# Optimization experiments

Hardware: AMD Instinct MI355X
Metric: run time of the kernel (lower is better)

Reference implementation:

```python
import jax, jax.numpy as jnp
import numpy as np

B, V, C, M, CM, D, OUT = 16, 16, 64, 32, 16, 128, 600
VOCAB = {"cond": 4000, "proc": 2000, "drug": 600, "lab_item": 700, "lab_value": 2000, "inj_item": 400, "inj_value": 2000}


def _gru(x, Wih, Whh, bih, bhh):
    """Batch-first torch-style GRU. x: [N,T,D] -> (outputs [N,T,D], h_T [N,D])."""
    Dh = Whh.shape[1]

    def step(h, xt):
        gi = xt @ Wih.T + bih
        gh = h @ Whh.T + bhh
        ir, iz, ig = jnp.split(gi, 3, axis=-1)
        hr, hz, hg = jnp.split(gh, 3, axis=-1)
        r = jax.nn.sigmoid(ir + hr)
        z = jax.nn.sigmoid(iz + hz)
        n = jnp.tanh(ig + r * hg)
        h = (1.0 - z) * n + z * h
        return h, h

    h0 = jnp.zeros((x.shape[0], Dh), x.dtype)
    hT, ys = jax.lax.scan(step, h0, jnp.swapaxes(x, 0, 1))
    return jnp.swapaxes(ys, 0, 1), hT


def _hetero_mp(feats, Wself, Wmsg):
    """Heterogeneous message passing over node types on the fully-connected
    monitor<->visit-feature bipartite pattern: each node type combines a self
    transform with a transformed mean of the other node types, then ReLU.
    feats: list of [N,D]; Wself/Wmsg: [T,D,D]."""
    stacked = jnp.stack(feats)  # [T,N,D]
    total = jnp.sum(stacked, axis=0)
    T = stacked.shape[0]
    outs = []
    for t in range(T):
        others = (total - stacked[t]) / (T - 1)
        outs.append(jax.nn.relu(stacked[t] @ Wself[t] + others @ Wmsg[t]))
    return outs


def _forward(codes_cond, codes_proc, codes_drug, codes_lab_item, codes_lab_value,
             codes_inj_item, codes_inj_value, weight, age,
             emb_cond, emb_proc, emb_drug, emb_lab_item, emb_lab_value,
             emb_inj_item, emb_inj_value,
             mgru_Wih, mgru_Whh, mgru_bih, mgru_bhh,
             vgru_Wih, vgru_Whh, vgru_bih, vgru_bhh,
             gnn_Wself, gnn_Wmsg,
             fc_weight_W, fc_weight_b, fc_age_W, fc_age_b,
             fc_patient_W, fc_patient_b):
    # ---- visit-event features: embedding lookup + sum-pool over codes ----
    vis = {}
    for k, codes, emb in (("cond", codes_cond, emb_cond),
                          ("proc", codes_proc, emb_proc),
                          ("drug", codes_drug, emb_drug)):
        vis[k] = jnp.sum(emb[codes], axis=2)  # [B,V,D]
    visit_keys = ("cond", "proc", "drug")

    # ---- monitor-event pairs: (item * value) embeddings, GNN, two-level GRU ----
    pairs = (
        (codes_lab_item, codes_lab_value, emb_lab_item, emb_lab_value, "lab_item", (0, 2, 3, 4)),
        (codes_inj_item, codes_inj_value, emb_inj_item, emb_inj_value, "inj_item", (1, 2, 3, 4)),
    )
    hid = {}
    for p, (ci, cv, ei, ev, ikey, gidx) in enumerate(pairs):
        mon = jnp.sum(ei[ci] * ev[cv], axis=3)  # [B,V,M,D]
        feats = [mon.reshape(-1, D)]  # monitor node type, [B*V*M, D]
        for k in visit_keys:  # visit features repeated across monitors
            feats.append(jnp.broadcast_to(vis[k][:, :, None, :], (B, V, M, D)).reshape(-1, D))
        outs = _hetero_mp(feats, gnn_Wself[p], gnn_Wmsg[p])
        for t, k in enumerate((ikey,) + visit_keys):
            g = gidx[t]
            # monitor-level GRU over the M monitors of each visit
            o, _ = _gru(outs[t].reshape(B * V, M, D), mgru_Wih[g], mgru_Whh[g], mgru_bih[g], mgru_bhh[g])
            last = o[:, -1, :].reshape(B, V, D)  # last monitor state per visit
            # visit-level GRU (source uses visit_gru[feature_key1] for all keys)
            _, h = _gru(last, vgru_Wih[p], vgru_Whh[p], vgru_bih[p], vgru_bhh[p])
            hid[k] = h if k not in hid else hid[k] + h

    # ---- weight / age scalar features ----
    for k, x, W, b, vi in (("weight", weight, fc_weight_W, fc_weight_b, 2),
                           ("age", age, fc_age_W, fc_age_b, 3)):
        mask = (x != 0.0)[..., None]  # [B,V,1]
        xe = (x[..., None] * W[:, 0] + b) * mask  # Linear(1->D) then zero-mask
        _, h = _gru(xe, vgru_Wih[vi], vgru_Whh[vi], vgru_bih[vi], vgru_bhh[vi])
        hid[k] = h

    # ---- concat in dict-insertion order, then ReLU + Linear head ----
    pe = jnp.concatenate([hid["lab_item"], hid["cond"], hid["proc"], hid["drug"],
                          hid["inj_item"], hid["weight"], hid["age"]], axis=-1)  # [B, 7D]
    return jax.nn.relu(pe) @ fc_patient_W.T + fc_patient_b  # [B, OUT]


def setup_inputs() -> dict:
    key = jax.random.key(0)
    ks = iter(jax.random.split(key, 64))

    def nrm(shape, s=0.1):
        return (jax.random.normal(next(ks), shape) * s).astype(jnp.float32)

    def emb_table(vsz):
        t = nrm((vsz, D), 1.0)
        return t.at[0].set(0.0)  # padding_idx=0 row is zero

    inp = {}
    inp["codes_cond"] = jax.random.randint(next(ks), (B, V, C), 0, VOCAB["cond"], dtype=jnp.int32)
    inp["codes_proc"] = jax.random.randint(next(ks), (B, V, C), 0, VOCAB["proc"], dtype=jnp.int32)
    inp["codes_drug"] = jax.random.randint(next(ks), (B, V, C), 0, VOCAB["drug"], dtype=jnp.int32)
    inp["codes_lab_item"] = jax.random.randint(next(ks), (B, V, M, CM), 0, VOCAB["lab_item"], dtype=jnp.int32)
    inp["codes_lab_value"] = jax.random.randint(next(ks), (B, V, M, CM), 0, VOCAB["lab_value"], dtype=jnp.int32)
    inp["codes_inj_item"] = jax.random.randint(next(ks), (B, V, M, CM), 0, VOCAB["inj_item"], dtype=jnp.int32)
    inp["codes_inj_value"] = jax.random.randint(next(ks), (B, V, M, CM), 0, VOCAB["inj_value"], dtype=jnp.int32)
    inp["weight"] = jax.random.uniform(next(ks), (B, V), minval=0.1, maxval=1.0, dtype=jnp.float32)
    inp["age"] = jax.random.uniform(next(ks), (B, V), minval=0.1, maxval=1.0, dtype=jnp.float32)
    inp["emb_cond"] = emb_table(VOCAB["cond"])
    inp["emb_proc"] = emb_table(VOCAB["proc"])
    inp["emb_drug"] = emb_table(VOCAB["drug"])
    inp["emb_lab_item"] = emb_table(VOCAB["lab_item"])
    inp["emb_lab_value"] = emb_table(VOCAB["lab_value"])
    inp["emb_inj_item"] = emb_table(VOCAB["inj_item"])
    inp["emb_inj_value"] = emb_table(VOCAB["inj_value"])
    inp["mgru_Wih"] = nrm((5, 3 * D, D))
    inp["mgru_Whh"] = nrm((5, 3 * D, D))
    inp["mgru_bih"] = nrm((5, 3 * D))
    inp["mgru_bhh"] = nrm((5, 3 * D))
    inp["vgru_Wih"] = nrm((4, 3 * D, D))
    inp["vgru_Whh"] = nrm((4, 3 * D, D))
    inp["vgru_bih"] = nrm((4, 3 * D))
    inp["vgru_bhh"] = nrm((4, 3 * D))
    inp["gnn_Wself"] = nrm((2, 4, D, D))
    inp["gnn_Wmsg"] = nrm((2, 4, D, D))
    inp["fc_weight_W"] = nrm((D, 1))
    inp["fc_weight_b"] = nrm((D,))
    inp["fc_age_W"] = nrm((D, 1))
    inp["fc_age_b"] = nrm((D,))
    inp["fc_patient_W"] = nrm((OUT, 7 * D))
    inp["fc_patient_b"] = nrm((OUT,))
    return inp


def reference(codes_cond, codes_proc, codes_drug, codes_lab_item, codes_lab_value,
              codes_inj_item, codes_inj_value, weight, age,
              emb_cond, emb_proc, emb_drug, emb_lab_item, emb_lab_value,
              emb_inj_item, emb_inj_value,
              mgru_Wih, mgru_Whh, mgru_bih, mgru_bhh,
              vgru_Wih, vgru_Whh, vgru_bih, vgru_bhh,
              gnn_Wself, gnn_Wmsg,
              fc_weight_W, fc_weight_b, fc_age_W, fc_age_b,
              fc_patient_W, fc_patient_b):
    return _forward(codes_cond, codes_proc, codes_drug, codes_lab_item, codes_lab_value,
                    codes_inj_item, codes_inj_value, weight, age,
                    emb_cond, emb_proc, emb_drug, emb_lab_item, emb_lab_value,
                    emb_inj_item, emb_inj_value,
                    mgru_Wih, mgru_Whh, mgru_bih, mgru_bhh,
                    vgru_Wih, vgru_Whh, vgru_bih, vgru_bhh,
                    gnn_Wself, gnn_Wmsg,
                    fc_weight_W, fc_weight_b, fc_age_W, fc_age_b,
                    fc_patient_W, fc_patient_b)
```

## Files before the change

### kernel.cpp

```cpp
#include <hip/hip_runtime.h>
#include <math.h>

#define B_   16
#define V_   16
#define C_   64
#define M_   32
#define CM_  16
#define D_   128
#define OUT_ 600
#define NSEQ 256
#define NROW 8192

typedef __attribute__((ext_vector_type(8))) short bf16x8;
typedef __attribute__((ext_vector_type(4))) short bf16x4;
typedef __attribute__((ext_vector_type(4))) float f32x4;

__device__ __forceinline__ unsigned short f2bf(float x) {
  union { float f; unsigned u; } v; v.f = x;
  unsigned r = v.u + 0x7fff + ((v.u >> 16) & 1);
  return (unsigned short)(r >> 16);
}
__device__ __forceinline__ float bf2f(short s) {
  union { unsigned u; float f; } v;
  v.u = ((unsigned)(unsigned short)s) << 16;
  return v.f;
}
__device__ __forceinline__ float fsig(float x)  { return __fdividef(1.f, 1.f + __expf(-x)); }
__device__ __forceinline__ float ftanh(float x) { return 1.f - 2.f*__fdividef(1.f, __expf(2.f*x) + 1.f); }

__device__ __forceinline__ void ldsbar() {
  asm volatile("s_waitcnt lgkmcnt(0)" ::: "memory");
  __builtin_amdgcn_s_barrier();
  asm volatile("" ::: "memory");
}

constexpr int OFF_VISB  = 98304;
constexpr int OFF_MONB  = 147456;
constexpr int OFF_W12T  = 2244608;
constexpr int OFF_WIHB  = 2375680;
constexpr int OFF_WIHTV = 2498560;
constexpr int OFF_XE    = 2695168;
constexpr int OFF_LAST  = 27926528;
constexpr int OFF_VH    = 29171712;

__global__ __launch_bounds__(256) void k_prepvis(
    const float* __restrict__ Wself, const float* __restrict__ Wmsg,
    const float* __restrict__ mWih,  const float* __restrict__ vWih,
    const float* __restrict__ wgt,   const float* __restrict__ age,
    const float* __restrict__ fwW,   const float* __restrict__ fwB,
    const float* __restrict__ faW,   const float* __restrict__ faB,
    const int* __restrict__ cc, const int* __restrict__ cp, const int* __restrict__ cd,
    const float* __restrict__ ec, const float* __restrict__ ep, const float* __restrict__ ed,
    const int* __restrict__ cli, const int* __restrict__ clv,
    const int* __restrict__ cii, const int* __restrict__ civ,
    const float* __restrict__ eli, const float* __restrict__ elv,
    const float* __restrict__ eii, const float* __restrict__ eiv,
    short* __restrict__ w12t, short* __restrict__ wihb,
    float* __restrict__ wihTv, float* __restrict__ xe,
    short* __restrict__ visb, short* __restrict__ monb)
{
  int bx = blockIdx.x, tid = threadIdx.x;
  if (bx < 1024) {
    int lin = bx*256 + tid;
    int pt = lin >> 15, rem = lin & 32767;
    int n = rem >> 8, k = rem & 255;
    float v;
    if (k < 128) v = Wself[pt*16384 + k*128 + n] - Wmsg[pt*16384 + k*128 + n]*(1.f/3.f);
    else         v = Wmsg[pt*16384 + (k-128)*128 + n]*(1.f/3.f);
    w12t[lin] = (short)f2bf(v);
  } else if (bx < 1984) {
    int lin = (bx-1024)*256 + tid;
    wihb[lin] = (short)f2bf(mWih[lin]);
  } else if (bx < 2752) {
    int lin = (bx-1984)*256 + tid;
    int g = lin / 49152, rem2 = lin % 49152;
    int k = rem2 / 384, j = rem2 % 384;
    wihTv[lin] = vWih[g*49152 + j*128 + k];
  } else if (bx < 3008) {
    int lin = (bx-2752)*256 + tid;
    int which = lin >> 15, rem2 = lin & 32767;
    int n = rem2 >> 7, d = rem2 & 127;
    float x  = which ? age[n] : wgt[n];
    float Wv = which ? faW[d] : fwW[d];
    float bb = which ? faB[d] : fwB[d];
    xe[lin] = (x != 0.0f) ? (x*Wv + bb) : 0.0f;
  } else if (bx < 3392) {
    int idx = (bx-3008)*256 + tid;
    int type = idx >> 15;
    int r = idx & 32767;
    int bv = r >> 7, d = r & 127;
    const int*   codes = (type==0) ? cc : (type==1) ? cp : cd;
    const float* emb   = (type==0) ? ec : (type==1) ? ep : ed;
    float acc = 0.f;
    for (int c = 0; c < C_; ++c) {
      int code = codes[bv*C_ + c];
      acc += emb[code*D_ + d];
    }
    visb[(type*NSEQ + bv)*D_ + d] = (short)f2bf(acc);
  } else {
    int rowid = (bx-3392)*2 + (tid >> 7);
    int p = rowid >> 13, bvm = rowid & 8191;
    int d = tid & 127;
    const int* ci = p ? cii : cli;  const int* cv = p ? civ : clv;
    const float* ei = p ? eii : eli; const float* ev = p ? eiv : elv;
    float acc = 0.f;
    #pragma unroll
    for (int c2 = 0; c2 < CM_; ++c2) {
      int iv = ci[bvm*CM_ + c2];
      int vv = cv[bvm*CM_ + c2];
      acc += ei[iv*D_ + d] * ev[vv*D_ + d];
    }
    monb[((size_t)p*NROW + bvm)*D_ + d] = (short)f2bf(acc);
  }
}

__global__ __launch_bounds__(512, 1) void k_ggru(
    const short* __restrict__ monb, const short* __restrict__ visb,
    const short* __restrict__ w12t, const short* __restrict__ wihb,
    const float* __restrict__ mWhh, const float* __restrict__ mbih,
    const float* __restrict__ mbhh, float* __restrict__ last)
{
  const int run  = blockIdx.x >> 4;
  const int pair = blockIdx.x & 15;
  const int p = run >> 2, t = run & 3;
  const int g = (run % 4 == 0) ? (run / 4) : (run % 4 + 1);
  const int tid = threadIdx.x;
  const int w = tid >> 6;
  const int lane = tid & 63;
  const int c = lane & 15, q = lane >> 4;
  const int j = w*16 + c;

  __shared__ short hb[2][4][16][40];
  __shared__ __align__(16) short Ys[2][16][136];
  __shared__ __align__(16) short Xl[2][4096];

  for (int idx = tid; idx < 2*4*16*40; idx += 512)
    ((short*)hb)[idx] = 0;

  bf16x8 bW12[8];
  #pragma unroll
  for (int kt = 0; kt < 8; ++kt)
    bW12[kt] = *(const bf16x8*)(w12t + (size_t)run*32768 + (size_t)(w*16+c)*256 + kt*32 + q*8);

  bf16x8 bWih[3][4];
  #pragma unroll
  for (int gate = 0; gate < 3; ++gate)
    #pragma unroll
    for (int kt = 0; kt < 4; ++kt)
      bWih[gate][kt] = *(const bf16x8*)(wihb + ((size_t)g*384 + gate*128 + j)*128 + kt*32 + q*8);

  bf16x8 bWhh[3][4];
  #pragma unroll
  for (int gate = 0; gate < 3; ++gate) {
    const float* wp = mWhh + ((size_t)g*384 + gate*128 + j)*128 + q*8;
    #pragma unroll
    for (int kt = 0; kt < 4; ++kt) {
      float4 lo = *(const float4*)(wp + kt*32);
      float4 hi = *(const float4*)(wp + kt*32 + 4);
      bf16x8 tt;
      tt[0]=(short)f2bf(lo.x); tt[1]=(short)f2bf(lo.y); tt[2]=(short)f2bf(lo.z); tt[3]=(short)f2bf(lo.w);
      tt[4]=(short)f2bf(hi.x); tt[5]=(short)f2bf(hi.y); tt[6]=(short)f2bf(hi.z); tt[7]=(short)f2bf(hi.w);
      bWhh[gate][kt] = tt;
    }
  }
  const float bs0 = mbih[g*384 +       j] + mbhh[g*384 +       j];
  const float bs1 = mbih[g*384 + 128 + j] + mbhh[g*384 + 128 + j];
  const float bi2 = mbih[g*384 + 256 + j];
  const float bh2 = mbhh[g*384 + 256 + j];

  const int xr_ = tid >> 5, xu = tid & 31;
  const int bv = pair*16 + xr_;
  const bool istot = (xu >= 16);
  const short* fsrc;
  int fstride;
  float vsf[8] = {0.f,0.f,0.f,0.f,0.f,0.f,0.f,0.f};
  if (!istot) {
    if (t == 0) { fsrc = monb + ((size_t)p*NROW + (size_t)bv*32)*128 + xu*8; fstride = 128; }
    else        { fsrc = visb + ((size_t)(t-1)*NSEQ + bv)*128 + xu*8;        fstride = 0;   }
  } else {
    fsrc = monb + ((size_t)p*NROW + (size_t)bv*32)*128 + (xu-16)*8;          fstride = 128;
    #pragma unroll
    for (int i = 0; i < 8; ++i)
      vsf[i] = bf2f(visb[(0*NSEQ + bv)*128 + (xu-16)*8 + i])
             + bf2f(visb[(1*NSEQ + bv)*128 + (xu-16)*8 + i])
             + bf2f(visb[(2*NSEQ + bv)*128 + (xu-16)*8 + i]);
  }
  auto fixtot = [&](bf16x8 x) -> bf16x8 {
    if (istot) {
      #pragma unroll
      for (int i = 0; i < 8; ++i) x[i] = (short)f2bf(bf2f(x[i]) + vsf[i]);
    }
    return x;
  };
  const int xdofs = xr_*256 + (((xu*16) ^ ((xr_&7)<<4)) >> 1);
  short* xdst0 = &Xl[0][xdofs];
  short* xdst1 = &Xl[1][xdofs];

  {
    bf16x8 x0 = fixtot(*(const bf16x8*)fsrc);
    bf16x8 x1 = fixtot(*(const bf16x8*)(fsrc + fstride));
    *(bf16x8*)xdst0 = x0;
    *(bf16x8*)xdst1 = x1;
  }
  float hf[4] = {0.f,0.f,0.f,0.f};
  const int ktw = w >> 1;
  const int kkw = (w & 1)*16 + c;
  ldsbar();

  {
    const char* xbase = (const char*)&Xl[0][0];
    f32x4 accY = (f32x4){0.f,0.f,0.f,0.f};
    #pragma unroll
    for (int kt = 0; kt < 8; ++kt) {
      bf16x8 aX = *(const bf16x8*)(xbase + c*512 + ((kt*64 + q*16) ^ ((c&7)<<4)));
      accY = __builtin_amdgcn_mfma_f32_16x16x32_bf16(aX, bW12[kt], accY, 0, 0, 0);
    }
    #pragma unroll
    for (int reg = 0; reg < 4; ++reg)
      Ys[0][q*4 + reg][w*16 + c] = (short)f2bf(fmaxf(accY[reg], 0.f));
  }
  ldsbar();

  #pragma unroll 1
  for (int m = 0; m < 32; ++m) {
    const int cur = m & 1, nxt = cur ^ 1;

    bf16x8 xnext;
    if (m < 30) xnext = *(const bf16x8*)(fsrc + (size_t)(m+2)*fstride);

    f32x4 accY = (f32x4){0.f,0.f,0.f,0.f};
    if (m < 31) {
      const char* xbase = (const char*)&Xl[nxt][0];
      #pragma unroll
      for (int kt = 0; kt < 8; ++kt) {
        bf16x8 aX = *(const bf16x8*)(xbase + c*512 + ((kt*64 + q*16) ^ ((c&7)<<4)));
        accY = __builtin_amdgcn_mfma_f32_16x16x32_bf16(aX, bW12[kt], accY, 0, 0, 0);
      }
    }

    bf16x8 ah[4], a2[4];
    #pragma unroll
    for (int kt = 0; kt < 4; ++kt) {
      ah[kt] = *(const bf16x8*)&hb[cur][kt][c][q*8];
      a2[kt] = *(const bf16x8*)&Ys[cur][c][kt*32 + q*8];
    }
    f32x4 acc0 = (f32x4){0.f,0.f,0.f,0.f};
    f32x4 acc1 = (f32x4){0.f,0.f,0.f,0.f};
    f32x4 aG2  = (f32x4){0.f,0.f,0.f,0.f};
    f32x4 aH2  = (f32x4){0.f,0.f,0.f,0.f};
    #pragma unroll
    for (int kt = 0; kt < 4; ++kt) {
      acc0 = __builtin_amdgcn_mfma_f32_16x16x32_bf16(ah[kt], bWhh[0][kt], acc0, 0, 0, 0);
      acc1 = __builtin_amdgcn_mfma_f32_16x16x32_bf16(ah[kt], bWhh[1][kt], acc1, 0, 0, 0);
      aH2  = __builtin_amdgcn_mfma_f32_16x16x32_bf16(ah[kt], bWhh[2][kt], aH2,  0, 0, 0);
    }
    #pragma unroll
    for (int kt = 0; kt < 4; ++kt) {
      acc0 = __builtin_amdgcn_mfma_f32_16x16x32_bf16(a2[kt], bWih[0][kt], acc0, 0, 0, 0);
      acc1 = __builtin_amdgcn_mfma_f32_16x16x32_bf16(a2[kt], bWih[1][kt], acc1, 0, 0, 0);
      aG2  = __builtin_amdgcn_mfma_f32_16x16x32_bf16(a2[kt], bWih[2][kt], aG2,  0, 0, 0);
    }

    if (m < 31) {
      #pragma unroll
      for (int reg = 0; reg < 4; ++reg)
        Ys[nxt][q*4 + reg][w*16 + c] = (short)f2bf(fmaxf(accY[reg], 0.f));
    }
    if (m < 30) *(bf16x8*)(cur ? xdst1 : xdst0) = fixtot(xnext);

    #pragma unroll
    for (int reg = 0; reg < 4; ++reg) {
      float rr = fsig(acc0[reg] + bs0);
      float zz = fsig(acc1[reg] + bs1);
      float nn = ftanh(aG2[reg] + bi2 + rr*(aH2[reg] + bh2));
      float hnew = (1.f - zz)*nn + zz*hf[reg];
      hf[reg] = hnew;
      hb[nxt][ktw][q*4 + reg][kkw] = (short)f2bf(hnew);
    }
    ldsbar();
  }

  #pragma unroll
  for (int reg = 0; reg < 4; ++reg)
    last[((size_t)run*NSEQ + pair*16 + q*4 + reg)*D_ + j] = hf[reg];
}

__global__ __launch_bounds__(768) void k_vgru(
    const float* __restrict__ last, const float* __restrict__ xe,
    const float* __restrict__ wihTv, const float* __restrict__ vbih,
    const float* __restrict__ vWhh, const float* __restrict__ vbhh,
    float* __restrict__ vh)
{
  int run = blockIdx.x >> 4, b = blockIdx.x & 15;
  int tid = threadIdx.x;
  int vidx = (run < 4) ? 0 : (run < 8) ? 1 : (run - 6);

  __shared__ float Xs[16][128];
  __shared__ float giL[16*384];
  __shared__ __align__(16) float hsv[128];
  __shared__ float gh[384];

  const float* X = (run < 8) ? (last + ((size_t)run*NSEQ + b*16)*D_)
                             : (xe + ((size_t)(run-8)*NSEQ + b*16)*D_);
  for (int idx = tid; idx < 2048; idx += 768)
    ((float*)Xs)[idx] = X[idx];
  if (tid < 128) hsv[tid] = 0.f;
  __syncthreads();

  {
    int half = (tid >= 384) ? 1 : 0;
    int j = tid - half*384;
    float accv[8];
    float bias = vbih[vidx*384 + j];
    #pragma unroll
    for (int s = 0; s < 8; ++s) accv[s] = bias;
    const float* W = wihTv + vidx*49152 + j;
    #pragma unroll 4
    for (int k = 0; k < 128; ++k) {
      float wv = W[k*384];
      #pragma unroll
      for (int s = 0; s < 8; ++s) accv[s] += Xs[half*8 + s][k] * wv;
    }
    #pragma unroll
    for (int s = 0; s < 8; ++s)
      giL[(half*8 + s)*384 + j] = accv[s];
  }

  int j = tid >> 1, kh = tid & 1;
  float w[64];
  const float4* wrow = (const float4*)(vWhh + (vidx*384 + j)*128 + kh*64);
  #pragma unroll
  for (int k4 = 0; k4 < 16; ++k4) {
    float4 t4 = wrow[k4];
    w[4*k4] = t4.x; w[4*k4+1] = t4.y; w[4*k4+2] = t4.z; w[4*k4+3] = t4.w;
  }
  float bj = vbhh[vidx*384 + j];
  __syncthreads();

  #pragma unroll 1
  for (int v = 0; v < 16; ++v) {
    const float4* h4 = (const float4*)(hsv + kh*64);
    float p0 = 0.f, p1 = 0.f;
    #pragma unroll
    for (int k4 = 0; k4 < 8; ++k4) {
      float4 u0 = h4[k4], u1 = h4[k4+8];
      p0 += w[4*k4   ]*u0.x + w[4*k4+1 ]*u0.y + w[4*k4+2 ]*u0.z + w[4*k4+3 ]*u0.w;
      p1 += w[4*k4+32]*u1.x + w[4*k4+33]*u1.y + w[4*k4+34]*u1.z + w[4*k4+35]*u1.w;
    }
    float part = p0 + p1;
    part += __shfl_xor(part, 1);
    if (kh == 0) gh[j] = bj + ((j < 256) ? giL[v*384 + j] : 0.f) + part;
    __syncthreads();
    if (tid < 128) {
      float r = fsig(gh[tid]);
      float z = fsig(gh[tid+128]);
      float gin = giL[v*384 + 256 + tid];
      float n = ftanh(gin + r*gh[tid+256]);
      hsv[tid] = (1.f - z)*n + z*hsv[tid];
    }
    __syncthreads();
  }
  if (tid < 128) vh[(run*16 + b)*D_ + tid] = hsv[tid];
}

__global__ __launch_bounds__(256) void k_head(
    const float* __restrict__ vh, const float* __restrict__ Wp,
    const float* __restrict__ bp, float* __restrict__ out)
{
  const int o = blockIdx.x;
  const int tid = threadIdx.x;
  const int b = tid & 15, kc = tid >> 4;
  const int a1[7] = {0,1,2,3,4,8,9};
  const int a2[7] = {-1,5,6,7,-1,-1,-1};
  const float4* wb = (const float4*)(Wp + (size_t)o*896 + kc*56);
  float acc = 0.f;
  #pragma unroll
  for (int i = 0; i < 14; ++i) {
    int cc2 = kc*56 + i*4;
    int s = cc2 >> 7, d0 = cc2 & 127;
    float4 a = *(const float4*)(vh + (a1[s]*16 + b)*D_ + d0);
    int s2 = a2[s];
    if (s2 >= 0) {
      float4 a2v = *(const float4*)(vh + (s2*16 + b)*D_ + d0);
      a.x += a2v.x; a.y += a2v.y; a.z += a2v.z; a.w += a2v.w;
    }
    a.x = fmaxf(a.x, 0.f); a.y = fmaxf(a.y, 0.f);
    a.z = fmaxf(a.z, 0.f); a.w = fmaxf(a.w, 0.f);
    float4 ww = wb[i];
    acc += a.x*ww.x + a.y*ww.y + a.z*ww.z + a.w*ww.w;
  }
  __shared__ float red[16][17];
  red[kc][b] = acc;
  __syncthreads();
  if (tid < 16) {
    float s = 0.f;
    #pragma unroll
    for (int k = 0; k < 16; ++k) s += red[k][tid];
    out[tid*OUT_ + o] = s + bp[o];
  }
}

extern "C" void kernel_launch(void* const* d_in, const int* in_sizes, int n_in,
                              void* d_out, int out_size, void* d_ws, size_t ws_size,
                              hipStream_t stream)
{
  (void)in_sizes; (void)n_in; (void)out_size; (void)ws_size;
  const int*   cc   = (const int*)  d_in[0];
  const int*   cp   = (const int*)  d_in[1];
  const int*   cd   = (const int*)  d_in[2];
  const int*   cli  = (const int*)  d_in[3];
  const int*   clv  = (const int*)  d_in[4];
  const int*   cii  = (const int*)  d_in[5];
  const int*   civ  = (const int*)  d_in[6];
  const float* wgt  = (const float*)d_in[7];
  const float* age  = (const float*)d_in[8];
  const float* ec   = (const float*)d_in[9];
  const float* ep   = (const float*)d_in[10];
  const float* ed   = (const float*)d_in[11];
  const float* eli  = (const float*)d_in[12];
  const float* elv  = (const float*)d_in[13];
  const float* eii  = (const float*)d_in[14];
  const float* eiv  = (const float*)d_in[15];
  const float* mWih = (const float*)d_in[16];
  const float* mWhh = (const float*)d_in[17];
  const float* mbih = (const float*)d_in[18];
  const float* mbhh = (const float*)d_in[19];
  const float* vWih = (const float*)d_in[20];
  const float* vWhh = (const float*)d_in[21];
  const float* vbih = (const float*)d_in[22];
  const float* vbhh = (const float*)d_in[23];
  const float* Wself= (const float*)d_in[24];
  const float* Wmsg = (const float*)d_in[25];
  const float* fwW  = (const float*)d_in[26];
  const float* fwB  = (const float*)d_in[27];
  const float* faW  = (const float*)d_in[28];
  const float* faB  = (const float*)d_in[29];
  const float* Wp   = (const float*)d_in[30];
  const float* bp   = (const float*)d_in[31];
  float* out = (float*)d_out;
  float* ws  = (float*)d_ws;

  short* visb  = (short*)(ws + OFF_VISB);
  short* monb  = (short*)(ws + OFF_MONB);
  short* w12t  = (short*)(ws + OFF_W12T);
  short* wihb  = (short*)(ws + OFF_WIHB);
  float* wihTv = ws + OFF_WIHTV;
  float* xe    = ws + OFF_XE;
  float* last  = ws + OFF_LAST;
  float* vh    = ws + OFF_VH;

  k_prepvis<<<11584, 256, 0, stream>>>(Wself, Wmsg, mWih, vWih, wgt, age,
                                       fwW, fwB, faW, faB,
                                       cc, cp, cd, ec, ep, ed,
                                       cli, clv, cii, civ, eli, elv, eii, eiv,
                                       w12t, wihb, wihTv, xe, visb, monb);
  k_ggru<<<128, 512, 0, stream>>>(monb, visb, w12t, wihb,
                                  mWhh, mbih, mbhh, last);
  k_vgru<<<160, 768, 0, stream>>>(last, xe, wihTv, vbih, vWhh, vbhh, vh);
  k_head<<<600, 256, 0, stream>>>(vh, Wp, bp, out);
}
```

Baseline: 251.3 us.

## Hoist time-invariant visit-feature GEMM terms out of monitor GRU loop

The per-step input projection splits into a part that depends on the monitor row and a part from visit features that stays fixed over the 32 steps. The fixed part (visit sum times the message weights, plus the self term when the target is a visit type) is now computed once into a precomputed accumulator before the loop. Each step then runs a K=128 MFMA over only the monitor row instead of K=256, and only half the threads stage X into a half-sized LDS buffer. In exchange, the t==0 run loads its own Wself weights from global memory as strided fp32 reads at startup, and rounding changes slightly because bf16 sums are formed differently.

```diff
diff --git a/kernel.cpp b/kernel.cpp
--- a/kernel.cpp
+++ b/kernel.cpp
@@ -117,8 +117,9 @@
 __global__ __launch_bounds__(512, 1) void k_ggru(
     const short* __restrict__ monb, const short* __restrict__ visb,
     const short* __restrict__ w12t, const short* __restrict__ wihb,
-    const float* __restrict__ mWhh, const float* __restrict__ mbih,
-    const float* __restrict__ mbhh, float* __restrict__ last)
+    const float* __restrict__ Wself, const float* __restrict__ mWhh,
+    const float* __restrict__ mbih, const float* __restrict__ mbhh,
+    float* __restrict__ last)
 {
   const int run  = blockIdx.x >> 4;
   const int pair = blockIdx.x & 15;
@@ -132,7 +133,7 @@
 
   __shared__ short hb[2][4][16][40];
   __shared__ __align__(16) short Ys[2][16][136];
-  __shared__ __align__(16) short Xl[2][4096];
+  __shared__ __align__(16) short Xl[2][2048];
 
   for (int idx = tid; idx < 2*4*16*40; idx += 512)
     ((short*)hb)[idx] = 0;
@@ -140,7 +141,48 @@
   bf16x8 bW12[8];
   #pragma unroll
   for (int kt = 0; kt < 8; ++kt)
-    bW12[kt] = *(const bf16x8*)(w12t + (size_t)run*32768 + (size_t)(w*16+c)*256 + kt*32 + q*8);
+    bW12[kt] = *(const bf16x8*)(w12t + (size_t)run*32768 + (size_t)j*256 + kt*32 + q*8);
+
+  bf16x8 bWs[4];
+  if (t == 0) {
+    const float* wsp = Wself + (size_t)run*16384 + j;
+    #pragma unroll
+    for (int kt = 0; kt < 4; ++kt) {
+      bf16x8 tt;
+      #pragma unroll
+      for (int i = 0; i < 8; ++i)
+        tt[i] = (short)f2bf(wsp[(kt*32 + q*8 + i)*128]);
+      bWs[kt] = tt;
+    }
+  } else {
+    #pragma unroll
+    for (int kt = 0; kt < 4; ++kt) bWs[kt] = bW12[kt+4];
+  }
+
+  f32x4 Cpre = (f32x4){0.f,0.f,0.f,0.f};
+  {
+    const int bvc = pair*16 + c;
+    #pragma unroll
+    for (int kt = 0; kt < 4; ++kt) {
+      const int ko = kt*32 + q*8;
+      bf16x8 v0 = *(const bf16x8*)(visb + (size_t)(0*NSEQ + bvc)*128 + ko);
+      bf16x8 v1 = *(const bf16x8*)(visb + (size_t)(1*NSEQ + bvc)*128 + ko);
+      bf16x8 v2 = *(const bf16x8*)(visb + (size_t)(2*NSEQ + bvc)*128 + ko);
+      bf16x8 vs;
+      #pragma unroll
+      for (int i = 0; i < 8; ++i)
+        vs[i] = (short)f2bf(bf2f(v0[i]) + bf2f(v1[i]) + bf2f(v2[i]));
+      Cpre = __builtin_amdgcn_mfma_f32_16x16x32_bf16(vs, bW12[kt+4], Cpre, 0, 0, 0);
+    }
+    if (t > 0) {
+      #pragma unroll
+      for (int kt = 0; kt < 4; ++kt) {
+        const int ko = kt*32 + q*8;
+        bf16x8 fv = *(const bf16x8*)(visb + (size_t)((t-1)*NSEQ + bvc)*128 + ko);
+        Cpre = __builtin_amdgcn_mfma_f32_16x16x32_bf16(fv, bW12[kt], Cpre, 0, 0, 0);
+      }
+    }
+  }
 
   bf16x8 bWih[3][4];
   #pragma unroll
@@ -168,39 +210,17 @@
   const float bi2 = mbih[g*384 + 256 + j];
   const float bh2 = mbhh[g*384 + 256 + j];
 
-  const int xr_ = tid >> 5, xu = tid & 31;
+  const bool stg = (tid < 256);
+  const int xr_ = (tid >> 4) & 15, xu = tid & 15;
   const int bv = pair*16 + xr_;
-  const bool istot = (xu >= 16);
-  const short* fsrc;
-  int fstride;
-  float vsf[8] = {0.f,0.f,0.f,0.f,0.f,0.f,0.f,0.f};
-  if (!istot) {
-    if (t == 0) { fsrc = monb + ((size_t)p*NROW + (size_t)bv*32)*128 + xu*8; fstride = 128; }
-    else        { fsrc = visb + ((size_t)(t-1)*NSEQ + bv)*128 + xu*8;        fstride = 0;   }
-  } else {
-    fsrc = monb + ((size_t)p*NROW + (size_t)bv*32)*128 + (xu-16)*8;          fstride = 128;
-    #pragma unroll
-    for (int i = 0; i < 8; ++i)
-      vsf[i] = bf2f(visb[(0*NSEQ + bv)*128 + (xu-16)*8 + i])
-             + bf2f(visb[(1*NSEQ + bv)*128 + (xu-16)*8 + i])
-             + bf2f(visb[(2*NSEQ + bv)*128 + (xu-16)*8 + i]);
-  }
-  auto fixtot = [&](bf16x8 x) -> bf16x8 {
-    if (istot) {
-      #pragma unroll
-      for (int i = 0; i < 8; ++i) x[i] = (short)f2bf(bf2f(x[i]) + vsf[i]);
-    }
-    return x;
-  };
-  const int xdofs = xr_*256 + (((xu*16) ^ ((xr_&7)<<4)) >> 1);
+  const short* fsrc = monb + ((size_t)p*NROW + (size_t)bv*32)*128 + xu*8;
+  const int xdofs = xr_*128 + (((xu*16) ^ ((xr_&7)<<4)) >> 1);
   short* xdst0 = &Xl[0][xdofs];
   short* xdst1 = &Xl[1][xdofs];
 
-  {
-    bf16x8 x0 = fixtot(*(const bf16x8*)fsrc);
-    bf16x8 x1 = fixtot(*(const bf16x8*)(fsrc + fstride));
-    *(bf16x8*)xdst0 = x0;
-    *(bf16x8*)xdst1 = x1;
+  if (stg) {
+    *(bf16x8*)xdst0 = *(const bf16x8*)fsrc;
+    *(bf16x8*)xdst1 = *(const bf16x8*)(fsrc + 128);
   }
   float hf[4] = {0.f,0.f,0.f,0.f};
   const int ktw = w >> 1;
@@ -209,11 +229,11 @@
 
   {
     const char* xbase = (const char*)&Xl[0][0];
-    f32x4 accY = (f32x4){0.f,0.f,0.f,0.f};
-    #pragma unroll
-    for (int kt = 0; kt < 8; ++kt) {
-      bf16x8 aX = *(const bf16x8*)(xbase + c*512 + ((kt*64 + q*16) ^ ((c&7)<<4)));
-      accY = __builtin_amdgcn_mfma_f32_16x16x32_bf16(aX, bW12[kt], accY, 0, 0, 0);
+    f32x4 accY = Cpre;
+    #pragma unroll
+    for (int kt = 0; kt < 4; ++kt) {
+      bf16x8 aX = *(const bf16x8*)(xbase + c*256 + ((kt*64 + q*16) ^ ((c&7)<<4)));
+      accY = __builtin_amdgcn_mfma_f32_16x16x32_bf16(aX, bWs[kt], accY, 0, 0, 0);
     }
     #pragma unroll
     for (int reg = 0; reg < 4; ++reg)
@@ -226,15 +246,15 @@
     const int cur = m & 1, nxt = cur ^ 1;
 
     bf16x8 xnext;
-    if (m < 30) xnext = *(const bf16x8*)(fsrc + (size_t)(m+2)*fstride);
-
-    f32x4 accY = (f32x4){0.f,0.f,0.f,0.f};
+    if (stg && m < 30) xnext = *(const bf16x8*)(fsrc + (size_t)(m+2)*128);
+
+    f32x4 accY = Cpre;
     if (m < 31) {
       const char* xbase = (const char*)&Xl[nxt][0];
       #pragma unroll
-      for (int kt = 0; kt < 8; ++kt) {
-        bf16x8 aX = *(const bf16x8*)(xbase + c*512 + ((kt*64 + q*16) ^ ((c&7)<<4)));
-        accY = __builtin_amdgcn_mfma_f32_16x16x32_bf16(aX, bW12[kt], accY, 0, 0, 0);
+      for (int kt = 0; kt < 4; ++kt) {
+        bf16x8 aX = *(const bf16x8*)(xbase + c*256 + ((kt*64 + q*16) ^ ((c&7)<<4)));
+        accY = __builtin_amdgcn_mfma_f32_16x16x32_bf16(aX, bWs[kt], accY, 0, 0, 0);
       }
     }
 
@@ -266,7 +286,7 @@
       for (int reg = 0; reg < 4; ++reg)
         Ys[nxt][q*4 + reg][w*16 + c] = (short)f2bf(fmaxf(accY[reg], 0.f));
     }
-    if (m < 30) *(bf16x8*)(cur ? xdst1 : xdst0) = fixtot(xnext);
+    if (stg && m < 30) *(bf16x8*)(cur ? xdst1 : xdst0) = xnext;
 
     #pragma unroll
     for (int reg = 0; reg < 4; ++reg) {
@@ -454,7 +474,7 @@
                                        cc, cp, cd, ec, ep, ed,
                                        cli, clv, cii, civ, eli, elv, eii, eiv,
                                        w12t, wihb, wihTv, xe, visb, monb);
-  k_ggru<<<128, 512, 0, stream>>>(monb, visb, w12t, wihb,
+  k_ggru<<<128, 512, 0, stream>>>(monb, visb, w12t, wihb, Wself,
                                   mWhh, mbih, mbhh, last);
   k_vgru<<<160, 768, 0, stream>>>(last, xe, wihTv, vbih, vWhh, vbhh, vh);
   k_head<<<600, 256, 0, stream>>>(vh, Wp, bp, out);
```

Result: faster. 244.8 us (-2.6%).
